# Optimization experiments

Measured on AMD Instinct MI355X. Metric: run time of the kernel, lower is better.

## Reference

```python
import jax, jax.numpy as jnp
import numpy as np
import math

WINDOW = 2048
EMBED = 1024
BATCH = 8


def setup_inputs() -> dict:
    key = jax.random.key(0)
    ks = jax.random.split(key, 7)
    s = 1.0 / math.sqrt(EMBED)
    return {
        "embeddings": jax.random.normal(ks[0], (BATCH, WINDOW, EMBED), dtype=jnp.float32),
        "Wq": jax.random.uniform(ks[1], (EMBED, EMBED), jnp.float32, -s, s),
        "bq": jax.random.uniform(ks[2], (EMBED,), jnp.float32, -s, s),
        "Wk": jax.random.uniform(ks[3], (EMBED, EMBED), jnp.float32, -s, s),
        "bk": jax.random.uniform(ks[4], (EMBED,), jnp.float32, -s, s),
        "Wv": jax.random.uniform(ks[5], (EMBED, EMBED), jnp.float32, -s, s),
        "bv": jax.random.uniform(ks[6], (EMBED,), jnp.float32, -s, s),
    }


def reference(embeddings, Wq, bq, Wk, bk, Wv, bv):
    # Linear layers: x @ W.T + b (torch nn.Linear convention)
    Q = jnp.einsum('bse,fe->bsf', embeddings, Wq) + bq
    K = jnp.einsum('bse,fe->bsf', embeddings, Wk) + bk
    V = jnp.einsum('bse,fe->bsf', embeddings, Wv) + bv
    scale = 1.0 / math.sqrt(EMBED)
    # [B, S, S] score matrix: A[b, i, j] = Q_i . K_j / sqrt(d)
    A = jnp.einsum('bie,bje->bij', Q, K) * scale
    # causal additive mask: -inf where j > i (strictly upper triangular)
    mask = jnp.triu(jnp.full((WINDOW, WINDOW), -jnp.inf, dtype=A.dtype), k=1)
    A = A + mask
    # NOTE: faithful to original nn.Softmax(dim=1): normalize over QUERY axis
    P = jax.nn.softmax(A, axis=1)
    return jnp.einsum('bij,bje->bie', P, V)
```

## Files before the change

kernel.cpp:

```cpp
#include <hip/hip_runtime.h>
#include <stdint.h>

#define WINDOW 2048
#define EMBED  1024
#define BATCH  8
#define MTOT   (BATCH*WINDOW)

typedef unsigned short u16;
typedef __bf16 bf16x8 __attribute__((ext_vector_type(8)));
typedef float  f32x4  __attribute__((ext_vector_type(4)));

#define BK 64
#define KSCALE 0.04508422717564447f

#define BM2 256
#define BN2 256
#define HALF2 8192
#define PLD  260

#define AHALFR 4096
#define BHALFR 8192

#define WAITVM4 asm volatile("s_waitcnt vmcnt(4)" ::: "memory")
#define WAITVM3 asm volatile("s_waitcnt vmcnt(3)" ::: "memory")
#define WAITVM0 asm volatile("s_waitcnt vmcnt(0)" ::: "memory")
#define SBAR    __builtin_amdgcn_s_barrier()

__device__ __forceinline__ u16 f2bf(float f) {
  union { float f; unsigned u; } a; a.f = f;
  unsigned r = a.u + 0x7FFF + ((a.u >> 16) & 1);
  return (u16)(r >> 16);
}
__device__ __forceinline__ float bf2f(u16 u) {
  union { unsigned u; float f; } a; a.u = ((unsigned)u) << 16;
  return a.f;
}

__device__ __forceinline__ void gload16(const u16* g, u16* l) {
  __builtin_amdgcn_global_load_lds(
      (const __attribute__((address_space(1))) unsigned int*)g,
      (__attribute__((address_space(3))) unsigned int*)l, 16, 0, 0);
}


__device__ __forceinline__ void gemm256(
    const u16* __restrict__ A, int lda,
    const u16* __restrict__ B, int ldb,
    int nt, u16* lds, f32x4 acc[8][4])
{
  const int tid  = threadIdx.x;
  const int lane = tid & 63;
  const int wid  = tid >> 6;
  const int wm   = (wid >> 2) * 128;
  const int wn   = (wid & 3) * 64;
  const int lrow = lane & 15;
  const int hi   = lane >> 4;
  u16* dA = lds;
  u16* dB = lds + 4 * HALF2;

  int aoff[8], boff[4];
  #pragma unroll
  for (int mi = 0; mi < 8; ++mi) {
    int r = wm + mi * 16 + lrow;
    aoff[mi] = r * 32 + ((hi ^ ((r >> 1) & 3)) << 3);
  }
  #pragma unroll
  for (int ni = 0; ni < 4; ++ni) {
    int r = wn + ni * 16 + lrow;
    boff[ni] = r * 32 + ((hi ^ ((r >> 1) & 3)) << 3);
  }

  const int f0 = tid, f1 = 512 + tid;
  const int r0 = f0 >> 2, r1 = f1 >> 2;
  const int c0 = (((f0 & 3) ^ ((r0 >> 1) & 3)) << 3);
  const int c1 = (((f1 & 3) ^ ((r1 >> 1) & 3)) << 3);
  const u16* pA0 = A + (size_t)r0 * lda + c0;
  const u16* pA1 = A + (size_t)r1 * lda + c1;
  const u16* pB0 = B + (size_t)r0 * ldb + c0;
  const u16* pB1 = B + (size_t)r1 * ldb + c1;
  const int d0 = f0 * 8, d1 = f1 * 8;

  gload16(pA0,      dA + d0);         gload16(pA1,      dA + d1);
  gload16(pB0,      dB + d0);         gload16(pB1,      dB + d1);
  gload16(pA0 + 32, dA + HALF2 + d0); gload16(pA1 + 32, dA + HALF2 + d1);
  gload16(pB0 + 32, dB + HALF2 + d0); gload16(pB1 + 32, dB + HALF2 + d1);
  pA0 += BK; pA1 += BK; pB0 += BK; pB1 += BK;
  WAITVM4;
  SBAR;

  for (int t = 0; t < nt; ++t) {
    const int cb = (t & 1) * 2;
    const int nb = ((t + 1) & 1) * 2;
    u16* LA0 = dA + cb * HALF2;  u16* LA1 = LA0 + HALF2;
    u16* LB0 = dB + cb * HALF2;  u16* LB1 = LB0 + HALF2;
    const bool s = (t + 1) < nt;
    bf16x8 av[8], bv[4];

    #pragma unroll
    for (int mi = 0; mi < 8; ++mi) av[mi] = *(const bf16x8*)(LA0 + aoff[mi]);
    #pragma unroll
    for (int ni = 0; ni < 4; ++ni) bv[ni] = *(const bf16x8*)(LB0 + boff[ni]);
    if (s) {
      gload16(pA0, dA + nb * HALF2 + d0); gload16(pA1, dA + nb * HALF2 + d1);
      gload16(pB0, dB + nb * HALF2 + d0); gload16(pB1, dB + nb * HALF2 + d1);
    }
    __builtin_amdgcn_s_setprio(1);
    #pragma unroll
    for (int mi = 0; mi < 8; ++mi)
      #pragma unroll
      for (int ni = 0; ni < 4; ++ni)
        acc[mi][ni] = __builtin_amdgcn_mfma_f32_16x16x32_bf16(av[mi], bv[ni], acc[mi][ni], 0, 0, 0);
    __builtin_amdgcn_s_setprio(0);
    if (s) { WAITVM4; } else { WAITVM0; }
    SBAR;

    #pragma unroll
    for (int mi = 0; mi < 8; ++mi) av[mi] = *(const bf16x8*)(LA1 + aoff[mi]);
    #pragma unroll
    for (int ni = 0; ni < 4; ++ni) bv[ni] = *(const bf16x8*)(LB1 + boff[ni]);
    if (s) {
      gload16(pA0 + 32, dA + nb * HALF2 + HALF2 + d0); gload16(pA1 + 32, dA + nb * HALF2 + HALF2 + d1);
      gload16(pB0 + 32, dB + nb * HALF2 + HALF2 + d0); gload16(pB1 + 32, dB + nb * HALF2 + HALF2 + d1);
      pA0 += BK; pA1 += BK; pB0 += BK; pB1 += BK;
    }
    __builtin_amdgcn_s_setprio(1);
    #pragma unroll
    for (int mi = 0; mi < 8; ++mi)
      #pragma unroll
      for (int ni = 0; ni < 4; ++ni)
        acc[mi][ni] = __builtin_amdgcn_mfma_f32_16x16x32_bf16(av[mi], bv[ni], acc[mi][ni], 0, 0, 0);
    __builtin_amdgcn_s_setprio(0);
    if (s) { WAITVM4; }
    SBAR;
  }
}

__device__ __forceinline__ void gemm_rect(
    const u16* __restrict__ A, int lda,
    const u16* __restrict__ B, int ldb,
    int nt, u16* lds, f32x4 acc[4][4])
{
  const int tid  = threadIdx.x;
  const int lane = tid & 63;
  const int wid  = tid >> 6;
  const int wm   = (wid >> 2) * 64;
  const int wn   = (wid & 3) * 64;
  const int lrow = lane & 15;
  const int hi   = lane >> 4;
  u16* dA = lds;
  u16* dB = lds + 4 * AHALFR;

  int aoff[4], boff[4];
  #pragma unroll
  for (int mi = 0; mi < 4; ++mi) {
    int r = wm + mi * 16 + lrow;
    aoff[mi] = r * 32 + ((hi ^ ((r >> 1) & 3)) << 3);
  }
  #pragma unroll
  for (int ni = 0; ni < 4; ++ni) {
    int r = wn + ni * 16 + lrow;
    boff[ni] = r * 32 + ((hi ^ ((r >> 1) & 3)) << 3);
  }

  const int fa = tid;
  const int fb0 = tid, fb1 = 512 + tid;
  const int ra = fa >> 2, rb0 = fb0 >> 2, rb1 = fb1 >> 2;
  const int ca  = (((fa  & 3) ^ ((ra  >> 1) & 3)) << 3);
  const int cb0 = (((fb0 & 3) ^ ((rb0 >> 1) & 3)) << 3);
  const int cb1 = (((fb1 & 3) ^ ((rb1 >> 1) & 3)) << 3);
  const u16* pA  = A + (size_t)ra  * lda + ca;
  const u16* pB0 = B + (size_t)rb0 * ldb + cb0;
  const u16* pB1 = B + (size_t)rb1 * ldb + cb1;
  const int da = fa * 8, db0 = fb0 * 8, db1 = fb1 * 8;

  gload16(pA,       dA + da);
  gload16(pB0,      dB + db0);          gload16(pB1,      dB + db1);
  gload16(pA + 32,  dA + AHALFR + da);
  gload16(pB0 + 32, dB + BHALFR + db0); gload16(pB1 + 32, dB + BHALFR + db1);
  pA += BK; pB0 += BK; pB1 += BK;
  WAITVM3;
  SBAR;

  for (int t = 0; t < nt; ++t) {
    const int cb = (t & 1) * 2;
    const int nb = ((t + 1) & 1) * 2;
    u16* LA0 = dA + cb * AHALFR;  u16* LA1 = LA0 + AHALFR;
    u16* LB0 = dB + cb * BHALFR;  u16* LB1 = LB0 + BHALFR;
    const bool s = (t + 1) < nt;
    bf16x8 av[4], bv[4];

    #pragma unroll
    for (int mi = 0; mi < 4; ++mi) av[mi] = *(const bf16x8*)(LA0 + aoff[mi]);
    #pragma unroll
    for (int ni = 0; ni < 4; ++ni) bv[ni] = *(const bf16x8*)(LB0 + boff[ni]);
    if (s) {
      gload16(pA,  dA + nb * AHALFR + da);
      gload16(pB0, dB + nb * BHALFR + db0); gload16(pB1, dB + nb * BHALFR + db1);
    }
    __builtin_amdgcn_s_setprio(1);
    #pragma unroll
    for (int mi = 0; mi < 4; ++mi)
      #pragma unroll
      for (int ni = 0; ni < 4; ++ni)
        acc[mi][ni] = __builtin_amdgcn_mfma_f32_16x16x32_bf16(av[mi], bv[ni], acc[mi][ni], 0, 0, 0);
    __builtin_amdgcn_s_setprio(0);
    if (s) { WAITVM3; } else { WAITVM0; }
    SBAR;

    #pragma unroll
    for (int mi = 0; mi < 4; ++mi) av[mi] = *(const bf16x8*)(LA1 + aoff[mi]);
    #pragma unroll
    for (int ni = 0; ni < 4; ++ni) bv[ni] = *(const bf16x8*)(LB1 + boff[ni]);
    if (s) {
      gload16(pA + 32,  dA + nb * AHALFR + AHALFR + da);
      gload16(pB0 + 32, dB + nb * BHALFR + BHALFR + db0);
      gload16(pB1 + 32, dB + nb * BHALFR + BHALFR + db1);
      pA += BK; pB0 += BK; pB1 += BK;
    }
    __builtin_amdgcn_s_setprio(1);
    #pragma unroll
    for (int mi = 0; mi < 4; ++mi)
      #pragma unroll
      for (int ni = 0; ni < 4; ++ni)
        acc[mi][ni] = __builtin_amdgcn_mfma_f32_16x16x32_bf16(av[mi], bv[ni], acc[mi][ni], 0, 0, 0);
    __builtin_amdgcn_s_setprio(0);
    if (s) { WAITVM3; }
    SBAR;
  }
}

__global__ __launch_bounds__(256) void k_cvt(const float* __restrict__ in,
                                             u16* __restrict__ out, int n) {
  int i = (blockIdx.x * 256 + threadIdx.x) * 4;
  if (i >= n) return;
  float4 v = *(const float4*)(in + i);
  ushort4 o;
  o.x = f2bf(v.x); o.y = f2bf(v.y); o.z = f2bf(v.z); o.w = f2bf(v.w);
  *(ushort4*)(out + i) = o;
}

__global__ __launch_bounds__(256) void k_cvtw(const float* __restrict__ w0,
                                              const float* __restrict__ w1,
                                              const float* __restrict__ w2,
                                              u16* __restrict__ out) {
  const float* in = (blockIdx.y == 0) ? w0 : (blockIdx.y == 1) ? w1 : w2;
  u16* o = out + (size_t)blockIdx.y * EMBED * EMBED;
  int i = (blockIdx.x * 256 + threadIdx.x) * 4;
  float4 v = *(const float4*)(in + i);
  ushort4 r;
  r.x = f2bf(v.x); r.y = f2bf(v.y); r.z = f2bf(v.z); r.w = f2bf(v.w);
  *(ushort4*)(o + i) = r;
}

__global__ __launch_bounds__(512, 2) void k_qkv(
    const u16* __restrict__ Xb, const u16* __restrict__ Wb,
    const float* __restrict__ bq, const float* __restrict__ bk, const float* __restrict__ bv,
    u16* __restrict__ Q, u16* __restrict__ Ks, u16* __restrict__ V)
{
  __shared__ u16 lds[8 * HALF2];
  const int m0 = blockIdx.x * BM2;
  const int n0 = blockIdx.y * BN2;
  const int z  = blockIdx.z;
  const u16*   W    = Wb + (size_t)z * EMBED * EMBED;
  const float* bias = (z == 0) ? bq : (z == 1) ? bk : bv;
  u16* out          = (z == 0) ? Q  : (z == 1) ? Ks : V;
  const float scale = (z == 1) ? KSCALE : 1.0f;

  f32x4 acc[8][4];
  const f32x4 zz = {0.f,0.f,0.f,0.f};
  #pragma unroll
  for (int i = 0; i < 8; ++i) for (int j = 0; j < 4; ++j) acc[i][j] = zz;
  gemm256(Xb + (size_t)m0 * EMBED, EMBED, W + (size_t)n0 * EMBED, EMBED,
          EMBED / BK, lds, acc);

  const int lane = threadIdx.x & 63, wid = threadIdx.x >> 6;
  const int wm = (wid >> 2) * 128, wn = (wid & 3) * 64;
  const int lrow = lane & 15, hi = lane >> 4;
  #pragma unroll
  for (int mi = 0; mi < 8; ++mi)
    #pragma unroll
    for (int ni = 0; ni < 4; ++ni)
      #pragma unroll
      for (int rr = 0; rr < 4; ++rr) {
        int gm = m0 + wm + mi * 16 + hi * 4 + rr;
        int gn = n0 + wn + ni * 16 + lrow;
        out[(size_t)gm * EMBED + gn] = f2bf((acc[mi][ni][rr] + bias[gn]) * scale);
      }
}

__global__ __launch_bounds__(512, 2) void k_spd(
    const u16* __restrict__ Q, const u16* __restrict__ Ks,
    u16* __restrict__ P, float* __restrict__ D)
{
  __shared__ u16 lds[BM2 * PLD];
  const int sblk = blockIdx.x;

  if (sblk < 256) {
    const int xcd = sblk & 7;
    const int q   = sblk >> 3;
    int it = 0;
    while (q >= ((it + 1) * (it + 2)) / 2) ++it;
    const int jt = q - (it * (it + 1)) / 2;
    const int b  = (xcd - it) & 7;
    const int i0 = it * BM2;
    const int j0 = jt * BN2;

    const u16* A = Q  + (size_t)b * WINDOW * EMBED + (size_t)i0 * EMBED;
    const u16* B = Ks + (size_t)b * WINDOW * EMBED + (size_t)j0 * EMBED;
    f32x4 acc[8][4];
    const f32x4 zz = {0.f,0.f,0.f,0.f};
    #pragma unroll
    for (int i = 0; i < 8; ++i) for (int j = 0; j < 4; ++j) acc[i][j] = zz;
    gemm256(A, EMBED, B, EMBED, EMBED / BK, lds, acc);

    u16* Pb   = P + (size_t)b * WINDOW * WINDOW;
    float* Db = D + (size_t)b * WINDOW;
    const int tid  = threadIdx.x;
    const int lane = tid & 63, wid = tid >> 6;
    const int wm = (wid >> 2) * 128, wn = (wid & 3) * 64;
    const int lrow = lane & 15, hi = lane >> 4;

    #pragma unroll
    for (int ni = 0; ni < 4; ++ni) {
      int lj = wn + ni * 16 + lrow;
      float csum = 0.f;
      #pragma unroll
      for (int mi = 0; mi < 8; ++mi)
        #pragma unroll
        for (int rr = 0; rr < 4; ++rr) {
          int li = wm + mi * 16 + hi * 4 + rr;
          float p = ((i0 + li) >= (j0 + lj)) ? exp2f(acc[mi][ni][rr]) : 0.0f;
          lds[li * PLD + lj] = f2bf(p);
          csum += p;
        }
      csum += __shfl_xor(csum, 16, 64);
      csum += __shfl_xor(csum, 32, 64);
      if (hi == 0) atomicAdd(&Db[j0 + lj], csum);
    }
    __syncthreads();

    #pragma unroll
    for (int it2 = 0; it2 < 16; ++it2) {
      int f   = it2 * 512 + tid;
      int row = f >> 5;
      int c   = f & 31;
      bf16x8 v = *(const bf16x8*)(lds + row * PLD + c * 8);
      *(bf16x8*)(Pb + (size_t)(i0 + row) * WINDOW + j0 + c * 8) = v;
    }
  } else {
    const int ih   = sblk - 256;
    const int xcd  = ih & 7;
    const int h    = ih >> 3;
    const int jt   = 4 + (h >> 1);
    const int half = h & 1;
    const int it   = 7;
    const int b    = (xcd - it) & 7;
    const int i0   = it * BM2 + half * 128;
    const int j0   = jt * BN2;

    const u16* A = Q  + (size_t)b * WINDOW * EMBED + (size_t)i0 * EMBED;
    const u16* B = Ks + (size_t)b * WINDOW * EMBED + (size_t)j0 * EMBED;
    f32x4 acc[4][4];
    const f32x4 zz = {0.f,0.f,0.f,0.f};
    #pragma unroll
    for (int i = 0; i < 4; ++i) for (int j = 0; j < 4; ++j) acc[i][j] = zz;
    gemm_rect(A, EMBED, B, EMBED, EMBED / BK, lds, acc);

    u16* Pb   = P + (size_t)b * WINDOW * WINDOW;
    float* Db = D + (size_t)b * WINDOW;
    const int lane = threadIdx.x & 63, wid = threadIdx.x >> 6;
    const int wm = (wid >> 2) * 64, wn = (wid & 3) * 64;
    const int lrow = lane & 15, hi = lane >> 4;
    #pragma unroll
    for (int ni = 0; ni < 4; ++ni) {
      int gj = j0 + wn + ni * 16 + lrow;
      float csum = 0.f;
      #pragma unroll
      for (int mi = 0; mi < 4; ++mi)
        #pragma unroll
        for (int rr = 0; rr < 4; ++rr) {
          int gi = i0 + wm + mi * 16 + hi * 4 + rr;
          float p = (gi >= gj) ? exp2f(acc[mi][ni][rr]) : 0.0f;
          Pb[(size_t)gi * WINDOW + gj] = f2bf(p);
          csum += p;
        }
      csum += __shfl_xor(csum, 16, 64);
      csum += __shfl_xor(csum, 32, 64);
      if (hi == 0) atomicAdd(&Db[gj], csum);
    }
  }
}

__global__ __launch_bounds__(256) void k_vdt(
    const u16* __restrict__ V, const float* __restrict__ D, u16* __restrict__ Vdt)
{
  __shared__ u16 tile[64][68];
  const int j0 = blockIdx.x * 64, e0 = blockIdx.y * 64, b = blockIdx.z;
  const u16* Vb = V   + (size_t)b * WINDOW * EMBED;
  u16* Tb       = Vdt + (size_t)b * EMBED * WINDOW;
  const float* Db = D + (size_t)b * WINDOW;
  const int t = threadIdx.x;
  const int rr = t >> 4;
  const int cc = (t & 15) * 4;
  #pragma unroll
  for (int p = 0; p < 4; ++p) {
    int r = p * 16 + rr;
    *(uint2*)&tile[r][cc] = *(const uint2*)(Vb + (size_t)(j0 + r) * EMBED + e0 + cc);
  }
  __syncthreads();
  #pragma unroll
  for (int p = 0; p < 4; ++p) {
    int er = p * 16 + rr;
    ushort4 o;
    o.x = f2bf(bf2f(tile[cc + 0][er]) / Db[j0 + cc + 0]);
    o.y = f2bf(bf2f(tile[cc + 1][er]) / Db[j0 + cc + 1]);
    o.z = f2bf(bf2f(tile[cc + 2][er]) / Db[j0 + cc + 2]);
    o.w = f2bf(bf2f(tile[cc + 3][er]) / Db[j0 + cc + 3]);
    *(ushort4*)(Tb + (size_t)(e0 + er) * WINDOW + j0 + cc) = o;
  }
}

__global__ __launch_bounds__(512, 2) void k_out(
    const u16* __restrict__ P, const u16* __restrict__ Vdt, float* __restrict__ O)
{
  __shared__ u16 lds[8 * HALF2];
  const int s   = blockIdx.x;
  const int xcd = s & 7;
  const int q   = s >> 3;
  float* ObBase;
  const int lane = threadIdx.x & 63, wid = threadIdx.x >> 6;
  const int lrow = lane & 15, hi = lane >> 4;

  if (q < 32) {
    const int it  = 7 - (q >> 3);
    const int sub = q & 7;
    const int hb  = sub >> 2;
    const int et  = sub & 3;
    const int b   = (xcd - it) & 7;
    const int i0  = it * BM2 + (hb ? 0 : 128);
    const int e0  = et * BN2;
    const int nt  = hb ? (4 * it + 2) : (4 * it + 4);

    const u16* A = P   + (size_t)b * WINDOW * WINDOW + (size_t)i0 * WINDOW;
    const u16* B = Vdt + (size_t)b * EMBED * WINDOW  + (size_t)e0 * WINDOW;
    f32x4 acc[4][4];
    const f32x4 zz = {0.f,0.f,0.f,0.f};
    #pragma unroll
    for (int i = 0; i < 4; ++i) for (int j = 0; j < 4; ++j) acc[i][j] = zz;
    gemm_rect(A, WINDOW, B, WINDOW, nt, lds, acc);

    ObBase = O + (size_t)b * WINDOW * EMBED;
    const int wm = (wid >> 2) * 64, wn = (wid & 3) * 64;
    #pragma unroll
    for (int mi = 0; mi < 4; ++mi)
      #pragma unroll
      for (int ni = 0; ni < 4; ++ni)
        #pragma unroll
        for (int rr = 0; rr < 4; ++rr) {
          int gi = i0 + wm + mi * 16 + hi * 4 + rr;
          int ge = e0 + wn + ni * 16 + lrow;
          ObBase[(size_t)gi * EMBED + ge] = acc[mi][ni][rr];
        }
  } else {
    const int qq = q - 32;
    const int it = 3 - (qq >> 2);
    const int et = qq & 3;
    const int b  = (xcd - it) & 7;
    const int i0 = it * BM2;
    const int e0 = et * BN2;

    const u16* A = P   + (size_t)b * WINDOW * WINDOW + (size_t)i0 * WINDOW;
    const u16* B = Vdt + (size_t)b * EMBED * WINDOW  + (size_t)e0 * WINDOW;
    f32x4 acc[8][4];
    const f32x4 zz = {0.f,0.f,0.f,0.f};
    #pragma unroll
    for (int i = 0; i < 8; ++i) for (int j = 0; j < 4; ++j) acc[i][j] = zz;
    gemm256(A, WINDOW, B, WINDOW, 4 * (it + 1), lds, acc);

    ObBase = O + (size_t)b * WINDOW * EMBED;
    const int wm = (wid >> 2) * 128, wn = (wid & 3) * 64;
    #pragma unroll
    for (int mi = 0; mi < 8; ++mi)
      #pragma unroll
      for (int ni = 0; ni < 4; ++ni)
        #pragma unroll
        for (int rr = 0; rr < 4; ++rr) {
          int gi = i0 + wm + mi * 16 + hi * 4 + rr;
          int ge = e0 + wn + ni * 16 + lrow;
          ObBase[(size_t)gi * EMBED + ge] = acc[mi][ni][rr];
        }
  }
}

extern "C" void kernel_launch(void* const* d_in, const int* in_sizes, int n_in,
                              void* d_out, int out_size, void* d_ws, size_t ws_size,
                              hipStream_t stream) {
  const float* X  = (const float*)d_in[0];
  const float* Wq = (const float*)d_in[1];
  const float* bq = (const float*)d_in[2];
  const float* Wk = (const float*)d_in[3];
  const float* bk = (const float*)d_in[4];
  const float* Wv = (const float*)d_in[5];
  const float* bv = (const float*)d_in[6];
  float* O = (float*)d_out;

  char* ws = (char*)d_ws;
  size_t off = 0;
  auto alloc = [&](size_t bytes) -> void* {
    void* p = ws + off; off += (bytes + 255) & ~(size_t)255; return p;
  };
  u16*  Xb  = (u16*)alloc((size_t)MTOT * EMBED * 2);
  u16*  Wb  = (u16*)alloc((size_t)3 * EMBED * EMBED * 2);
  u16*  Qb  = (u16*)alloc((size_t)MTOT * EMBED * 2);
  u16*  Kb  = (u16*)alloc((size_t)MTOT * EMBED * 2);
  u16*  Vb  = (u16*)alloc((size_t)MTOT * EMBED * 2);
  u16*  Vdt = (u16*)alloc((size_t)BATCH * EMBED * WINDOW * 2);
  u16*  P   = (u16*)alloc((size_t)BATCH * WINDOW * WINDOW * 2);
  float* D  = (float*)alloc((size_t)MTOT * 4);
  (void)ws_size; (void)in_sizes; (void)n_in; (void)out_size;

  k_cvt<<<dim3((MTOT * EMBED / 4 + 255) / 256), 256, 0, stream>>>(X, Xb, MTOT * EMBED);
  k_cvtw<<<dim3(EMBED * EMBED / 4 / 256, 3), 256, 0, stream>>>(Wq, Wk, Wv, Wb);

  k_qkv<<<dim3(MTOT / BM2, EMBED / BN2, 3), 512, 0, stream>>>(Xb, Wb, bq, bk, bv, Qb, Kb, Vb);

  (void)hipMemsetAsync(D, 0, (size_t)MTOT * 4, stream);
  k_spd<<<dim3(320), 512, 0, stream>>>(Qb, Kb, P, D);

  k_vdt<<<dim3(WINDOW / 64, EMBED / 64, BATCH), 256, 0, stream>>>(Vb, D, Vdt);

  k_out<<<dim3(384), 512, 0, stream>>>(P, Vdt, O);
}
```

Baseline: 270.0 us.

## Move V projection GEMM into score kernel to fill idle tail blocks

The V projection is taken out of the QKV GEMM launch and computed by 256 extra blocks appended to the score/exp kernel, which grows from 320 to 576 blocks. The aim is to fill the tail imbalance of both kernels: the QKV launch shrinks from 3 to 2 output matrices, and the triangular score work shares the GPU with independent V tiles. The cost is a larger, heavier kernel whose scheduling and tail now depend on the block ordering.

Result: no change. 268.8 us (-0.5%).

```diff
diff --git a/kernel.cpp b/kernel.cpp
--- a/kernel.cpp
+++ b/kernel.cpp
@@ -254,16 +254,16 @@
 
 __global__ __launch_bounds__(512, 2) void k_qkv(
     const u16* __restrict__ Xb, const u16* __restrict__ Wb,
-    const float* __restrict__ bq, const float* __restrict__ bk, const float* __restrict__ bv,
-    u16* __restrict__ Q, u16* __restrict__ Ks, u16* __restrict__ V)
+    const float* __restrict__ bq, const float* __restrict__ bk,
+    u16* __restrict__ Q, u16* __restrict__ Ks)
 {
   __shared__ u16 lds[8 * HALF2];
   const int m0 = blockIdx.x * BM2;
   const int n0 = blockIdx.y * BN2;
   const int z  = blockIdx.z;
   const u16*   W    = Wb + (size_t)z * EMBED * EMBED;
-  const float* bias = (z == 0) ? bq : (z == 1) ? bk : bv;
-  u16* out          = (z == 0) ? Q  : (z == 1) ? Ks : V;
+  const float* bias = (z == 0) ? bq : bk;
+  u16* out          = (z == 0) ? Q  : Ks;
   const float scale = (z == 1) ? KSCALE : 1.0f;
 
   f32x4 acc[8][4];
@@ -288,9 +288,11 @@
       }
 }
 
-__global__ __launch_bounds__(512, 2) void k_spd(
+__global__ __launch_bounds__(512, 2) void k_spdv(
     const u16* __restrict__ Q, const u16* __restrict__ Ks,
-    u16* __restrict__ P, float* __restrict__ D)
+    const u16* __restrict__ Xb, const u16* __restrict__ Wb,
+    const float* __restrict__ bv,
+    u16* __restrict__ P, float* __restrict__ D, u16* __restrict__ Vb)
 {
   __shared__ u16 lds[BM2 * PLD];
   const int sblk = blockIdx.x;
@@ -347,7 +349,7 @@
       bf16x8 v = *(const bf16x8*)(lds + row * PLD + c * 8);
       *(bf16x8*)(Pb + (size_t)(i0 + row) * WINDOW + j0 + c * 8) = v;
     }
-  } else {
+  } else if (sblk < 320) {
     const int ih   = sblk - 256;
     const int xcd  = ih & 7;
     const int h    = ih >> 3;
@@ -388,6 +390,36 @@
       csum += __shfl_xor(csum, 32, 64);
       if (hi == 0) atomicAdd(&Db[gj], csum);
     }
+  } else {
+    const int v    = sblk - 320;
+    const int xcd  = v & 7;
+    const int g    = v >> 3;
+    const int mloc = g & 7;
+    const int nt4  = g >> 3;
+    const int m0   = (xcd * 8 + mloc) * BM2;
+    const int n0   = nt4 * BN2;
+    const u16* Wv  = Wb + (size_t)2 * EMBED * EMBED;
+
+    f32x4 acc[8][4];
+    const f32x4 zz = {0.f,0.f,0.f,0.f};
+    #pragma unroll
+    for (int i = 0; i < 8; ++i) for (int j = 0; j < 4; ++j) acc[i][j] = zz;
+    gemm256(Xb + (size_t)m0 * EMBED, EMBED, Wv + (size_t)n0 * EMBED, EMBED,
+            EMBED / BK, lds, acc);
+
+    const int lane = threadIdx.x & 63, wid = threadIdx.x >> 6;
+    const int wm = (wid >> 2) * 128, wn = (wid & 3) * 64;
+    const int lrow = lane & 15, hi = lane >> 4;
+    #pragma unroll
+    for (int mi = 0; mi < 8; ++mi)
+      #pragma unroll
+      for (int ni = 0; ni < 4; ++ni)
+        #pragma unroll
+        for (int rr = 0; rr < 4; ++rr) {
+          int gm = m0 + wm + mi * 16 + hi * 4 + rr;
+          int gn = n0 + wn + ni * 16 + lrow;
+          Vb[(size_t)gm * EMBED + gn] = f2bf(acc[mi][ni][rr] + bv[gn]);
+        }
   }
 }
 
@@ -522,10 +554,10 @@
   k_cvt<<<dim3((MTOT * EMBED / 4 + 255) / 256), 256, 0, stream>>>(X, Xb, MTOT * EMBED);
   k_cvtw<<<dim3(EMBED * EMBED / 4 / 256, 3), 256, 0, stream>>>(Wq, Wk, Wv, Wb);
 
-  k_qkv<<<dim3(MTOT / BM2, EMBED / BN2, 3), 512, 0, stream>>>(Xb, Wb, bq, bk, bv, Qb, Kb, Vb);
+  k_qkv<<<dim3(MTOT / BM2, EMBED / BN2, 2), 512, 0, stream>>>(Xb, Wb, bq, bk, Qb, Kb);
 
   (void)hipMemsetAsync(D, 0, (size_t)MTOT * 4, stream);
-  k_spd<<<dim3(320), 512, 0, stream>>>(Qb, Kb, P, D);
+  k_spdv<<<dim3(576), 512, 0, stream>>>(Qb, Kb, Xb, Wb, bv, P, D, Vb);
 
   k_vdt<<<dim3(WINDOW / 64, EMBED / 64, BATCH), 256, 0, stream>>>(Vb, D, Vdt);
 
```
